# Kernel tuning notes

Hardware: AMD Instinct MI355X
Metric: run time of the kernel (lower is better)

The kernel has to match this reference:

```python
import jax, jax.numpy as jnp
import numpy as np

B, S, I, H = 1_000_000, 1, 2, 1
SPIN, TRAIN = 10_000, 800_000


def setup_inputs() -> dict:
    key = jax.random.key(0)
    ks = jax.random.split(key, 9)
    return {
        "x": jax.random.normal(ks[0], (B, S, I), jnp.float32),
        "y_obs": jax.random.normal(ks[1], (B, H), jnp.float32),
        "weight_r_yom": jax.random.uniform(ks[2], (H, H), jnp.float32),
        "weight_r_ylm": jax.random.uniform(ks[3], (H, H), jnp.float32),
        "weight_r_yfm": jax.random.uniform(ks[4], (H, H), jnp.float32),
        "bias_b0_yom": jax.random.uniform(ks[5], (H,), jnp.float32),
        "weight_b1_yom": jax.random.uniform(ks[6], (H, H), jnp.float32),
        "bias_b0_ylm": jax.random.uniform(ks[7], (H,), jnp.float32),
        "weight_b2_ylm": jax.random.uniform(ks[8], (H, H), jnp.float32),
        "epoch": 1,
        "time_lag": 0,
    }


def reference(x, y_obs, weight_r_yom, weight_r_ylm, weight_r_yfm,
              bias_b0_yom, weight_b1_yom, bias_b0_ylm, weight_b2_ylm,
              epoch, time_lag):
    # x: [B, S, I] (batch_first). The torch code carries hidden state across
    # the b-loop, so b is the sequential recurrence axis. time_lag == 0 here,
    # so every step is processed (no zero-prefix masking needed).
    Bsz = x.shape[0]
    Hh = bias_b0_yom.shape[0]

    # Softmax-like gate scales over the three mass pathways (param-only, hoisted).
    e_o, e_l, e_f = jnp.exp(weight_r_yom), jnp.exp(weight_r_ylm), jnp.exp(weight_r_yfm)
    denom = e_o + e_l + e_f
    oo1 = e_o / denom  # [H, H]
    ol1 = e_l / denom  # [H, H]

    # torch.std is unbiased (ddof=1)
    obsstd = jnp.std(y_obs[SPIN:TRAIN], ddof=1)

    b0_yom = bias_b0_yom[None, :]  # [1, H]
    b0_ylm = bias_b0_ylm[None, :]  # [1, H]

    def t_step(c0, u):
        # c0: [1, H] cell state; u: [I] inputs at this step
        u1 = jnp.broadcast_to(u[0], (1, Hh))  # mass input
        u2 = jnp.broadcast_to(u[1], (1, Hh))  # aux forcing
        # mo=0, so=1, ml=0, sl=1 (no scaling variant)
        oo = oo1 * jax.nn.sigmoid(b0_yom + c0 @ weight_b1_yom)   # outflow gate
        ol = ol1 * jax.nn.sigmoid(b0_ylm + u2 @ weight_b2_ylm)   # loss gate
        f = 1.0 - oo - ol                                        # forget (mass-conserving)
        c1 = f * c0 + u1                                         # ib = 0 -> (1-ib)*g = u1
        h0 = oo * c0
        l0 = ol * c0
        return c1, (h0, c0, l0, oo, ol, f)

    def b_step(c0, xb):
        # xb: [S, I]; the torch code overwrites per-b outputs each t, so only
        # the last t's records survive.
        c1, recs = jax.lax.scan(t_step, c0, xb)
        last = jax.tree.map(lambda r: r[-1], recs)
        return c1, last

    c_init = jnp.zeros((1, Hh), x.dtype)
    _, (h0s, c0s, l0s, oos, ols, fs) = jax.lax.scan(b_step, c_init, x)

    rs = lambda a: a.reshape(Bsz, Hh)
    h_n, c_n, l_n = rs(h0s), rs(c0s), rs(l0s)
    Gate_oo, Gate_ol, Gate_f = rs(oos), rs(ols), rs(fs)
    zeros = jnp.zeros_like(h_n)  # bp_n and Gate_ib are identically 0 (ib = 0)
    obs_std = jnp.full_like(h_n, obsstd)
    h_nout = jnp.concatenate([h_n, obs_std], axis=1)
    return (h_n, c_n, l_n, zeros, zeros, Gate_oo, Gate_ol, Gate_f, h_nout, obs_std)
```

## Files before the change

### kernel.cpp

```cpp
#include <hip/hip_runtime.h>

#define BQ    1000000
#define SPIN  10000
#define TRAIN 800000
#define NOBS  (TRAIN - SPIN)
#define CHUNK 17
#define BLK_ELEMS (64 * CHUNK)
#define NBLK 920
#define LOOKBACK 192
#define XWIN (LOOKBACK + BLK_ELEMS)
#define RED_BLOCKS 256

__global__ __launch_bounds__(256) void std_partials_kernel(
    const float* __restrict__ y, double* __restrict__ ws) {
  const float4* y4 = (const float4*)(y + SPIN);
  const int NG = NOBS / 4;
  int tid = blockIdx.x * 256 + threadIdx.x;
  double s = 0.0, ss = 0.0;
  for (int g = tid; g < NG; g += RED_BLOCKS * 256) {
    float4 v = y4[g];
    double a = v.x, b = v.y, c = v.z, d = v.w;
    s += (a + b) + (c + d);
    ss += (a * a + b * b) + (c * c + d * d);
  }
  for (int off = 32; off > 0; off >>= 1) {
    s  += __shfl_down(s, off);
    ss += __shfl_down(ss, off);
  }
  __shared__ double sm[4][2];
  int wave = threadIdx.x >> 6;
  if ((threadIdx.x & 63) == 0) { sm[wave][0] = s; sm[wave][1] = ss; }
  __syncthreads();
  if (threadIdx.x == 0) {
    ws[2 * blockIdx.x]     = sm[0][0] + sm[1][0] + sm[2][0] + sm[3][0];
    ws[2 * blockIdx.x + 1] = sm[0][1] + sm[1][1] + sm[2][1] + sm[3][1];
  }
}

__global__ __launch_bounds__(64) void scan_kernel(
    const float2* __restrict__ x,
    const float* __restrict__ wr_yom, const float* __restrict__ wr_ylm,
    const float* __restrict__ wr_yfm, const float* __restrict__ b0_yom,
    const float* __restrict__ wb1_yom, const float* __restrict__ b0_ylm,
    const float* __restrict__ wb2_ylm,
    const double* __restrict__ ws, float* __restrict__ out) {
  __shared__ __align__(16) float xs[XWIN];
  __shared__ __align__(16) float ysh[XWIN];
  __shared__ __align__(16) float cbuf[BLK_ELEMS];
  const int l = threadIdx.x;
  const int R = blockIdx.x * BLK_ELEMS;

  float eo = __expf(wr_yom[0]);
  float el = __expf(wr_ylm[0]);
  float ef = __expf(wr_yfm[0]);
  float denom = eo + el + ef;
  float oo1 = eo / denom;
  float ol1 = el / denom;
  const float K2E = 1.44269504088896340736f;
  float a1 = -wb1_yom[0] * K2E, k1 = -b0_yom[0] * K2E;
  float a2 = -wb2_ylm[0] * K2E, k2 = -b0_ylm[0] * K2E;

  const int gbase = R - LOOKBACK;
#pragma unroll
  for (int k = 0; k < XWIN / 128; ++k) {
    int e = (k * 64 + l) * 2;
    int g = gbase + e;
    if (g >= 0 && g + 1 < BQ) {
      float4 v = *(const float4*)&x[g];
      xs[e] = v.x; ysh[e] = v.y; xs[e + 1] = v.z; ysh[e + 1] = v.w;
    } else {
#pragma unroll
      for (int j = 0; j < 2; ++j) {
        int gi = g + j;
        float2 v = (gi >= 0 && gi < BQ) ? x[gi] : make_float2(0.0f, 0.0f);
        xs[e + j] = v.x; ysh[e + j] = v.y;
      }
    }
  }

  double S = 0.0, SS = 0.0;
#pragma unroll
  for (int k = 0; k < 4; ++k) {
    S  += ws[2 * (l + 64 * k)];
    SS += ws[2 * (l + 64 * k) + 1];
  }
  for (int off = 32; off > 0; off >>= 1) {
    S  += __shfl_xor(S, off);
    SS += __shfl_xor(SS, off);
  }
  const float stdv =
      (float)sqrt((SS - S * S / (double)NOBS) / (double)(NOBS - 1));

  __syncthreads();

  const int s0 = R + CHUNK * l;
  if (s0 < BQ) {
    const int wsteps = min(LOOKBACK, s0);
    const int nmain = min(CHUNK, BQ - s0);
    float c = 0.0f;
    int idx = CHUNK * l + (LOOKBACK - wsteps);

#define STEP()                                                        \
    do {                                                              \
      float ux = xs[idx], uy = ysh[idx];                              \
      float r2 = __builtin_amdgcn_rcpf(                               \
          1.0f + __builtin_amdgcn_exp2f(fmaf(uy, a2, k2)));           \
      float r1 = __builtin_amdgcn_rcpf(                               \
          1.0f + __builtin_amdgcn_exp2f(fmaf(c, a1, k1)));            \
      float pre = fmaf(-ol1 * c, r2, c + ux);                         \
      c = fmaf(-oo1 * c, r1, pre);                                    \
      ++idx;                                                          \
    } while (0)

    if (wsteps == LOOKBACK && nmain == CHUNK) {
#pragma unroll 8
      for (int t = 0; t < LOOKBACK; ++t) STEP();
#pragma unroll
      for (int t = 0; t < CHUNK; ++t) { cbuf[CHUNK * l + t] = c; STEP(); }
    } else {
      for (int t = 0; t < wsteps; ++t) STEP();
      for (int t = 0; t < nmain; ++t) { cbuf[CHUNK * l + t] = c; STEP(); }
    }
#undef STEP
  }
  __syncthreads();

  const int ng = min(BLK_ELEMS, BQ - R) >> 2;
  const float4 z4 = {0.0f, 0.0f, 0.0f, 0.0f};
  const float4 s4 = {stdv, stdv, stdv, stdv};
  for (int i = l; i < ng; i += 64) {
    const int b0 = R + 4 * i;
    float4 c4 = *(const float4*)&cbuf[4 * i];
    float4 u4 = *(const float4*)&ysh[LOOKBACK + 4 * i];
    float cc[4] = {c4.x, c4.y, c4.z, c4.w};
    float u2[4] = {u4.x, u4.y, u4.z, u4.w};
    float hv[4], lv[4], oov[4], olv[4], fv[4];
#pragma unroll
    for (int e = 0; e < 4; ++e) {
      float ce = cc[e];
      float ol_ = ol1 * __builtin_amdgcn_rcpf(
          1.0f + __builtin_amdgcn_exp2f(fmaf(u2[e], a2, k2)));
      float oo_ = oo1 * __builtin_amdgcn_rcpf(
          1.0f + __builtin_amdgcn_exp2f(fmaf(ce, a1, k1)));
      hv[e] = oo_ * ce; lv[e] = ol_ * ce;
      oov[e] = oo_; olv[e] = ol_; fv[e] = 1.0f - oo_ - ol_;
    }
    *(float4*)(out + b0)          = make_float4(hv[0], hv[1], hv[2], hv[3]);
    *(float4*)(out + BQ + b0)     = c4;
    *(float4*)(out + 2 * BQ + b0) = make_float4(lv[0], lv[1], lv[2], lv[3]);
    *(float4*)(out + 3 * BQ + b0) = z4;
    *(float4*)(out + 4 * BQ + b0) = z4;
    *(float4*)(out + 5 * BQ + b0) = make_float4(oov[0], oov[1], oov[2], oov[3]);
    *(float4*)(out + 6 * BQ + b0) = make_float4(olv[0], olv[1], olv[2], olv[3]);
    *(float4*)(out + 7 * BQ + b0) = make_float4(fv[0], fv[1], fv[2], fv[3]);
    *(float4*)(out + 8 * BQ + 2 * b0)     = make_float4(hv[0], stdv, hv[1], stdv);
    *(float4*)(out + 8 * BQ + 2 * b0 + 4) = make_float4(hv[2], stdv, hv[3], stdv);
    *(float4*)(out + 10 * BQ + b0) = s4;
  }
}

extern "C" void kernel_launch(void* const* d_in, const int* in_sizes, int n_in,
                              void* d_out, int out_size, void* d_ws, size_t ws_size,
                              hipStream_t stream) {
  const float* x       = (const float*)d_in[0];
  const float* y_obs   = (const float*)d_in[1];
  const float* wr_yom  = (const float*)d_in[2];
  const float* wr_ylm  = (const float*)d_in[3];
  const float* wr_yfm  = (const float*)d_in[4];
  const float* b0_yom  = (const float*)d_in[5];
  const float* wb1_yom = (const float*)d_in[6];
  const float* b0_ylm  = (const float*)d_in[7];
  const float* wb2_ylm = (const float*)d_in[8];
  float* out = (float*)d_out;
  double* ws = (double*)d_ws;

  std_partials_kernel<<<RED_BLOCKS, 256, 0, stream>>>(y_obs, ws);

  scan_kernel<<<NBLK, 64, 0, stream>>>(
      (const float2*)x, wr_yom, wr_ylm, wr_yfm, b0_yom, wb1_yom, b0_ylm,
      wb2_ylm, ws, out);
}
```

Measured before the change: 109.8 us.

## Precompute input-driven loss gate into shared memory and shorten scan lookback

The loss gate depends only on the aux input, so it is now computed once per element during the shared-memory load as g = 1 - ol, and the recurrence step uses c*g + u minus the outflow term. This takes one exp/rcp pair per step out of the serial recurrence, including the lookback warm-up steps, and also out of the output phase. The lookback window drops from 192 to 128 steps, which cuts redundant warm-up work but relies on the recurrence forgetting its start state within fewer steps, so accuracy could suffer. The load loop gains a bounds break because the window is no longer a multiple of 128.

```diff
diff --git a/kernel.cpp b/kernel.cpp
--- a/kernel.cpp
+++ b/kernel.cpp
@@ -7,7 +7,7 @@
 #define CHUNK 17
 #define BLK_ELEMS (64 * CHUNK)
 #define NBLK 920
-#define LOOKBACK 192
+#define LOOKBACK 128
 #define XWIN (LOOKBACK + BLK_ELEMS)
 #define RED_BLOCKS 256
 
@@ -45,7 +45,7 @@
     const float* __restrict__ wb2_ylm,
     const double* __restrict__ ws, float* __restrict__ out) {
   __shared__ __align__(16) float xs[XWIN];
-  __shared__ __align__(16) float ysh[XWIN];
+  __shared__ __align__(16) float gs[XWIN];
   __shared__ __align__(16) float cbuf[BLK_ELEMS];
   const int l = threadIdx.x;
   const int R = blockIdx.x * BLK_ELEMS;
@@ -62,20 +62,24 @@
 
   const int gbase = R - LOOKBACK;
 #pragma unroll
-  for (int k = 0; k < XWIN / 128; ++k) {
+  for (int k = 0; k < (XWIN + 127) / 128; ++k) {
     int e = (k * 64 + l) * 2;
+    if (e >= XWIN) break;
     int g = gbase + e;
+    float2 v0, v1;
     if (g >= 0 && g + 1 < BQ) {
       float4 v = *(const float4*)&x[g];
-      xs[e] = v.x; ysh[e] = v.y; xs[e + 1] = v.z; ysh[e + 1] = v.w;
+      v0 = make_float2(v.x, v.y); v1 = make_float2(v.z, v.w);
     } else {
-#pragma unroll
-      for (int j = 0; j < 2; ++j) {
-        int gi = g + j;
-        float2 v = (gi >= 0 && gi < BQ) ? x[gi] : make_float2(0.0f, 0.0f);
-        xs[e + j] = v.x; ysh[e + j] = v.y;
-      }
+      v0 = (g >= 0 && g < BQ) ? x[g] : make_float2(0.0f, 0.0f);
+      v1 = (g + 1 >= 0 && g + 1 < BQ) ? x[g + 1] : make_float2(0.0f, 0.0f);
     }
+    xs[e]     = v0.x;
+    xs[e + 1] = v1.x;
+    gs[e]     = fmaf(-ol1, __builtin_amdgcn_rcpf(
+        1.0f + __builtin_amdgcn_exp2f(fmaf(v0.y, a2, k2))), 1.0f);
+    gs[e + 1] = fmaf(-ol1, __builtin_amdgcn_rcpf(
+        1.0f + __builtin_amdgcn_exp2f(fmaf(v1.y, a2, k2))), 1.0f);
   }
 
   double S = 0.0, SS = 0.0;
@@ -102,13 +106,12 @@
 
 #define STEP()                                                        \
     do {                                                              \
-      float ux = xs[idx], uy = ysh[idx];                              \
-      float r2 = __builtin_amdgcn_rcpf(                               \
-          1.0f + __builtin_amdgcn_exp2f(fmaf(uy, a2, k2)));           \
+      float ux = xs[idx], gg = gs[idx];                               \
       float r1 = __builtin_amdgcn_rcpf(                               \
           1.0f + __builtin_amdgcn_exp2f(fmaf(c, a1, k1)));            \
-      float pre = fmaf(-ol1 * c, r2, c + ux);                         \
-      c = fmaf(-oo1 * c, r1, pre);                                    \
+      float t = oo1 * c;                                              \
+      float p = fmaf(c, gg, ux);                                      \
+      c = fmaf(-t, r1, p);                                            \
       ++idx;                                                          \
     } while (0)
 
@@ -131,19 +134,18 @@
   for (int i = l; i < ng; i += 64) {
     const int b0 = R + 4 * i;
     float4 c4 = *(const float4*)&cbuf[4 * i];
-    float4 u4 = *(const float4*)&ysh[LOOKBACK + 4 * i];
+    float4 g4 = *(const float4*)&gs[LOOKBACK + 4 * i];
     float cc[4] = {c4.x, c4.y, c4.z, c4.w};
-    float u2[4] = {u4.x, u4.y, u4.z, u4.w};
+    float gg[4] = {g4.x, g4.y, g4.z, g4.w};
     float hv[4], lv[4], oov[4], olv[4], fv[4];
 #pragma unroll
     for (int e = 0; e < 4; ++e) {
       float ce = cc[e];
-      float ol_ = ol1 * __builtin_amdgcn_rcpf(
-          1.0f + __builtin_amdgcn_exp2f(fmaf(u2[e], a2, k2)));
       float oo_ = oo1 * __builtin_amdgcn_rcpf(
           1.0f + __builtin_amdgcn_exp2f(fmaf(ce, a1, k1)));
+      float ol_ = 1.0f - gg[e];
       hv[e] = oo_ * ce; lv[e] = ol_ * ce;
-      oov[e] = oo_; olv[e] = ol_; fv[e] = 1.0f - oo_ - ol_;
+      oov[e] = oo_; olv[e] = ol_; fv[e] = gg[e] - oo_;
     }
     *(float4*)(out + b0)          = make_float4(hv[0], hv[1], hv[2], hv[3]);
     *(float4*)(out + BQ + b0)     = c4;
```

New measurement: 102.5 us (median of 2 runs). 1.07x faster.
